# Optimization experiments

Hardware: AMD Instinct MI355X
Metric: run time of the kernel (lower is better)

## Reference

```python
import jax, jax.numpy as jnp
import numpy as np

RHO = 0.5
SIGMA = 0.3
BATCH = 32768
L = 1024

# Concrete drifts (abstract in the original base class): classic linear filtering pair
# b(x, y) = -x  (mean-reverting state drift), B(x, y) = x (observation drift = state)
def _b(x, y):
    return -x

def _B(x, y):
    return x


def setup_inputs() -> dict:
    key = jax.random.key(0)
    k1, k2, k3 = jax.random.split(key, 3)
    x0 = jax.random.normal(k1, (BATCH,), dtype=jnp.float32)
    y0 = jax.random.normal(k2, (BATCH,), dtype=jnp.float32)
    ts = (jnp.arange(L, dtype=jnp.float32) / (L - 1))  # uniform grid on [0, 1]
    z = jax.random.normal(k3, (L - 1, BATCH, 2), dtype=jnp.float32)
    return {"x0": x0, "y0": y0, "ts": ts, "z": z}


def reference(x0, y0, ts, z):
    hs = ts[1:] - ts[:-1]  # (L-1,)

    def step(carry, inp):
        x, y = carry
        h, zi = inp  # h scalar, zi (batch, 2)
        sqrt_h = jnp.sqrt(h)
        dW1 = sqrt_h * zi[:, 1]
        # faithful to source: dW[:,0] = rho^2*dW[:,0] + (1-rho^2)*dW[:,1]
        dW0 = RHO ** 2 * (sqrt_h * zi[:, 0]) + (1.0 - RHO ** 2) * dW1
        x_new = x + _b(x, y) * h + SIGMA * dW0
        # note: source updates x first, then uses the NEW x inside B
        y_new = y + _B(x_new, y) * h + dW1
        return (x_new, y_new), jnp.stack((x_new, y_new), axis=1)  # (batch, 2)

    (_, _), traj = jax.lax.scan(step, (x0, y0), (hs, z))  # traj: (L-1, batch, 2)
    xy0 = jnp.stack((x0, y0), axis=1)[None]  # (1, batch, 2)
    xy = jnp.concatenate([xy0, traj], axis=0)  # (L, batch, 2)
    return jnp.transpose(xy, (1, 0, 2))  # (batch, L, 2)
```

## Files before the change

kernel.cpp:

```cpp
#include <hip/hip_runtime.h>

#define BATCH 32768
#define LEN   1024
#define TT    16
#define NTK   64
#define WV    8
#define PB    128

typedef float f32x4 __attribute__((ext_vector_type(4)));


__global__ __launch_bounds__(512, 2)
void sde_kernel(const float* __restrict__ x0,
                const float* __restrict__ y0,
                const float* __restrict__ ts,
                const float* __restrict__ z,
                float* __restrict__ out)
{
    const int tid  = threadIdx.x;
    const int lane = tid & 63;
    const int w    = tid >> 6;
    const int bb   = blockIdx.x * PB;

    __shared__ __align__(16) float2 ttile[WV][PB][18];
    __shared__ __align__(16) float2 arr[WV][PB];

    const float h  = (ts[LEN - 1] - ts[0]) * (1.0f / 1023.0f);
    const float q  = 1.0f - h;
    const float sh = sqrtf(h);
    const float Ax = 0.075f * sh;
    const float Bx = 0.225f * sh;
    const float q2 = q * q, q4 = q2 * q2, q8 = q4 * q4;
    const float ALPHA = q8 * q8;
    const float GAL   = q * (1.0f - ALPHA);
    const float l2q   = log2f(q);

    const int off = blockIdx.x & 7;
    const int NR  = off ? 9 : 8;

    const float2 xi = *(const float2*)&x0[bb + 2 * lane];
    const float2 yi = *(const float2*)&y0[bb + 2 * lane];

    const int   jloc = (2 * lane) & 15;
    const float a0 = exp2f((float)(jloc + 1) * l2q);
    const float a1 = a0 * q;
    const float g0 = q * (1.0f - a0);
    const float g1 = q * (1.0f - a1);
    const int   wt = lane >> 3;

    const float4* zb4 = (const float4*)z + (bb >> 1) + lane;

    float U0 = 0.f, V0 = 0.f, U1 = 0.f, V1 = 0.f;

    for (int r = 0; r < NR; ++r) {
        const int  k  = 8 * r + w - off;
        const bool kv = (unsigned)k < (unsigned)NTK;

        if (kv) {
            float4 zv[TT];
            const int rowb = 16 * k - 1;
#pragma unroll
            for (int j = 0; j < TT; ++j) {
                int row = rowb + j;
                row = row < 0 ? 0 : row;
                zv[j] = zb4[(size_t)row << 14];
            }
            float xa, ya, xb, yb;
            if (k == 0) { xa = xi.x; ya = yi.x; xb = xi.y; yb = yi.y; }
            else        { xa = 0.f;  ya = 0.f;  xb = 0.f;  yb = 0.f;  }
#pragma unroll
            for (int j = 0; j < TT; j += 2) {
                float2 pa0, pb0;
                if (j == 0 && k == 0) {
                    pa0 = make_float2(xa, ya); pb0 = make_float2(xb, yb);
                } else {
                    const float4 zi = zv[j];
                    xa = fmaf(xa, q, fmaf(Ax, zi.x, Bx * zi.y));
                    ya = ya + fmaf(xa, h, sh * zi.y);
                    xb = fmaf(xb, q, fmaf(Ax, zi.z, Bx * zi.w));
                    yb = yb + fmaf(xb, h, sh * zi.w);
                    pa0 = make_float2(xa, ya); pb0 = make_float2(xb, yb);
                }
                const float4 zi1 = zv[j + 1];
                xa = fmaf(xa, q, fmaf(Ax, zi1.x, Bx * zi1.y));
                ya = ya + fmaf(xa, h, sh * zi1.y);
                xb = fmaf(xb, q, fmaf(Ax, zi1.z, Bx * zi1.w));
                yb = yb + fmaf(xb, h, sh * zi1.w);
                *(float4*)&ttile[w][2 * lane    ][j] = make_float4(pa0.x, pa0.y, xa, ya);
                *(float4*)&ttile[w][2 * lane + 1][j] = make_float4(pb0.x, pb0.y, xb, yb);
            }
            *(float4*)&arr[w][2 * lane] = make_float4(xa, ya, xb, yb);
        }

        __syncthreads();

        if (w == 0) {
#pragma unroll
            for (int wp = 0; wp < WV; ++wp) {
                const int kp = 8 * r + wp - off;
                if ((unsigned)kp < (unsigned)NTK) {
                    const float4 s = *(const float4*)&arr[wp][2 * lane];
                    *(float4*)&arr[wp][2 * lane] = make_float4(U0, V0, U1, V1);
                    const float nU0 = fmaf(ALPHA, U0, s.x);
                    V0 = s.y + V0 + GAL * U0;  U0 = nU0;
                    const float nU1 = fmaf(ALPHA, U1, s.z);
                    V1 = s.w + V1 + GAL * U1;  U1 = nU1;
                }
            }
        }

        __syncthreads();

        {
            const int  kw = 8 * r + wt - off;
            const bool lv = (unsigned)kw < (unsigned)NTK;
            if (lv) {
                const int colf = (8 * r - off) * 32 + 4 * lane;
#pragma unroll
                for (int i = 0; i < 16; ++i) {
                    const int p = w * 16 + i;
                    const float4 t  = *(const float4*)&ttile[wt][p][jloc];
                    const float2 uv = arr[wt][p];
                    f32x4 o;
                    o.x = fmaf(uv.x, a0, t.x);
                    o.y = t.y + uv.y + uv.x * g0;
                    o.z = fmaf(uv.x, a1, t.z);
                    o.w = t.w + uv.y + uv.x * g1;
                    __builtin_nontemporal_store(o,
                        (f32x4*)&out[(size_t)(bb + p) * 2048 + colf]);
                }
            }
        }

        __syncthreads();
    }
}

extern "C" void kernel_launch(void* const* d_in, const int* in_sizes, int n_in,
                              void* d_out, int out_size, void* d_ws, size_t ws_size,
                              hipStream_t stream) {
    const float* x0 = (const float*)d_in[0];
    const float* y0 = (const float*)d_in[1];
    const float* ts = (const float*)d_in[2];
    const float* z  = (const float*)d_in[3];
    float* out = (float*)d_out;
    (void)d_ws; (void)ws_size; (void)in_sizes; (void)n_in; (void)out_size;

    sde_kernel<<<BATCH / PB, 512, 0, stream>>>(x0, y0, ts, z, out);
}
```

Measured before the change: 98.80 us.

## Double-buffer z prefetch across rounds and swizzle the LDS trajectory tile

Unrolls the round loop into nine fixed macro invocations. Each round now issues the next round's z loads into a second register buffer before computing the current one. Barriers only wait on LDS counters, so those global loads stay in flight across synchronisation. The shared trajectory tile uses an XOR swizzle on the column index to reduce bank conflicts on the transposed reads. The cost is roughly double the register footprint for z, under a 512x2 launch bound, which risks spills or lower occupancy.

```diff
diff --git a/kernel.cpp b/kernel.cpp
--- a/kernel.cpp
+++ b/kernel.cpp
@@ -9,6 +9,87 @@
 
 typedef float f32x4 __attribute__((ext_vector_type(4)));
 
+
+#define BAR() do { asm volatile("s_waitcnt lgkmcnt(0)" ::: "memory"); \
+                   __builtin_amdgcn_s_barrier(); } while (0)
+
+#define STEP(ZI) do { \
+    xa = fmaf(xa, q, fmaf(Ax, ZI.x, Bx * ZI.y)); \
+    ya = ya + fmaf(xa, h, sh * ZI.y); \
+    xb = fmaf(xb, q, fmaf(Ax, ZI.z, Bx * ZI.w)); \
+    yb = yb + fmaf(xb, h, sh * ZI.w); \
+} while (0)
+
+#define ROUND(R, CUR, NXT, PRE_, FIRST_) do { \
+    const int k_ = 8 * (R) + w - off; \
+    if (PRE_) {   \
+        const int kn_ = 8 * ((R) + 1) + w - off;    \
+        if ((unsigned)kn_ < (unsigned)NTK) { \
+            const int rowb_ = 16 * kn_ - 1; \
+            _Pragma("unroll") \
+            for (int j = 0; j < TT; ++j) \
+                NXT[j] = zb4[(size_t)(rowb_ + j) << 14]; \
+        } \
+    } \
+    if ((unsigned)k_ < (unsigned)NTK) { \
+        float xa, ya, xb, yb; \
+        if (FIRST_ && k_ == 0) { xa = xi.x; ya = yi.x; xb = xi.y; yb = yi.y; } \
+        else                   { xa = 0.f;  ya = 0.f;  xb = 0.f;  yb = 0.f;  } \
+        float* tb0_ = ttile + ((size_t)w * PB + 2 * lane) * 36; \
+        _Pragma("unroll") \
+        for (int j = 0; j < TT; j += 2) { \
+            float2 pa0_, pb0_; \
+            if (FIRST_ && k_ == 0 && j == 0) { \
+                pa0_ = make_float2(xa, ya); pb0_ = make_float2(xb, yb); \
+            } else { \
+                const float4 zi_ = CUR[j]; STEP(zi_); \
+                pa0_ = make_float2(xa, ya); pb0_ = make_float2(xb, yb); \
+            } \
+            const float4 zi1_ = CUR[j + 1]; STEP(zi1_); \
+            const int o_ = 4 * ((j >> 1) ^ csw); \
+            *(float4*)&tb0_[o_]      = make_float4(pa0_.x, pa0_.y, xa, ya); \
+            *(float4*)&tb0_[36 + o_] = make_float4(pb0_.x, pb0_.y, xb, yb); \
+        } \
+        *(float4*)&arr[w][4 * lane] = make_float4(xa, ya, xb, yb); \
+    } \
+    BAR();   \
+    if (w == 0) { \
+        _Pragma("unroll") \
+        for (int wp = 0; wp < WV; ++wp) { \
+            const int kp_ = 8 * (R) + wp - off; \
+            if ((unsigned)kp_ < (unsigned)NTK) { \
+                const float4 s_ = *(const float4*)&arr[wp][4 * lane]; \
+                *(float4*)&arr[wp][4 * lane] = make_float4(U0, V0, U1, V1); \
+                const float nU0_ = fmaf(ALPHA, U0, s_.x); \
+                V0 = s_.y + V0 + GAL * U0;  U0 = nU0_; \
+                const float nU1_ = fmaf(ALPHA, U1, s_.z); \
+                V1 = s_.w + V1 + GAL * U1;  U1 = nU1_; \
+            } \
+        } \
+    } \
+    BAR();   \
+    { \
+        const int kw_ = 8 * (R) + wt - off; \
+        if ((unsigned)kw_ < (unsigned)NTK) { \
+            const int colf_ = (8 * (R) - off) * 32 + 4 * lane; \
+            _Pragma("unroll") \
+            for (int i = 0; i < 16; ++i) { \
+                const int p_ = w * 16 + i; \
+                const float4 t_ = *(const float4*)&ttile[ \
+                    ((size_t)wt * PB + p_) * 36 + 4 * (csw ^ ((p_ >> 1) & 7))]; \
+                const float2 uv_ = *(const float2*)&arr[wt][2 * p_]; \
+                f32x4 o_; \
+                o_.x = fmaf(uv_.x, a0, t_.x); \
+                o_.y = t_.y + uv_.y + uv_.x * g0; \
+                o_.z = fmaf(uv_.x, a1, t_.z); \
+                o_.w = t_.w + uv_.y + uv_.x * g1; \
+                __builtin_nontemporal_store(o_, \
+                    (f32x4*)&out[(size_t)(bb + p_) * 2048 + colf_]); \
+            } \
+        } \
+    } \
+    BAR();   \
+} while (0)
 
 __global__ __launch_bounds__(512, 2)
 void sde_kernel(const float* __restrict__ x0,
@@ -22,8 +103,8 @@
     const int w    = tid >> 6;
     const int bb   = blockIdx.x * PB;
 
-    __shared__ __align__(16) float2 ttile[WV][PB][18];
-    __shared__ __align__(16) float2 arr[WV][PB];
+    __shared__ __align__(16) float ttile[WV * PB * 36];
+    __shared__ __align__(16) float arr[WV][260];
 
     const float h  = (ts[LEN - 1] - ts[0]) * (1.0f / 1023.0f);
     const float q  = 1.0f - h;
@@ -33,16 +114,15 @@
     const float q2 = q * q, q4 = q2 * q2, q8 = q4 * q4;
     const float ALPHA = q8 * q8;
     const float GAL   = q * (1.0f - ALPHA);
-    const float l2q   = log2f(q);
 
     const int off = blockIdx.x & 7;
-    const int NR  = off ? 9 : 8;
 
     const float2 xi = *(const float2*)&x0[bb + 2 * lane];
     const float2 yi = *(const float2*)&y0[bb + 2 * lane];
 
+    const int   csw  = lane & 7;
     const int   jloc = (2 * lane) & 15;
-    const float a0 = exp2f((float)(jloc + 1) * l2q);
+    const float a0 = exp2f((float)(jloc + 1) * log2f(q));
     const float a1 = a0 * q;
     const float g0 = q * (1.0f - a0);
     const float g1 = q * (1.0f - a1);
@@ -52,88 +132,30 @@
 
     float U0 = 0.f, V0 = 0.f, U1 = 0.f, V1 = 0.f;
 
-    for (int r = 0; r < NR; ++r) {
-        const int  k  = 8 * r + w - off;
-        const bool kv = (unsigned)k < (unsigned)NTK;
+    float4 zvA[TT], zvB[TT];
 
-        if (kv) {
-            float4 zv[TT];
-            const int rowb = 16 * k - 1;
+    {
+        const int k0 = w - off;
+        if ((unsigned)k0 < (unsigned)NTK) {
+            const int rowb = 16 * k0 - 1;
 #pragma unroll
             for (int j = 0; j < TT; ++j) {
                 int row = rowb + j;
                 row = row < 0 ? 0 : row;
-                zv[j] = zb4[(size_t)row << 14];
-            }
-            float xa, ya, xb, yb;
-            if (k == 0) { xa = xi.x; ya = yi.x; xb = xi.y; yb = yi.y; }
-            else        { xa = 0.f;  ya = 0.f;  xb = 0.f;  yb = 0.f;  }
-#pragma unroll
-            for (int j = 0; j < TT; j += 2) {
-                float2 pa0, pb0;
-                if (j == 0 && k == 0) {
-                    pa0 = make_float2(xa, ya); pb0 = make_float2(xb, yb);
-                } else {
-                    const float4 zi = zv[j];
-                    xa = fmaf(xa, q, fmaf(Ax, zi.x, Bx * zi.y));
-                    ya = ya + fmaf(xa, h, sh * zi.y);
-                    xb = fmaf(xb, q, fmaf(Ax, zi.z, Bx * zi.w));
-                    yb = yb + fmaf(xb, h, sh * zi.w);
-                    pa0 = make_float2(xa, ya); pb0 = make_float2(xb, yb);
-                }
-                const float4 zi1 = zv[j + 1];
-                xa = fmaf(xa, q, fmaf(Ax, zi1.x, Bx * zi1.y));
-                ya = ya + fmaf(xa, h, sh * zi1.y);
-                xb = fmaf(xb, q, fmaf(Ax, zi1.z, Bx * zi1.w));
-                yb = yb + fmaf(xb, h, sh * zi1.w);
-                *(float4*)&ttile[w][2 * lane    ][j] = make_float4(pa0.x, pa0.y, xa, ya);
-                *(float4*)&ttile[w][2 * lane + 1][j] = make_float4(pb0.x, pb0.y, xb, yb);
-            }
-            *(float4*)&arr[w][2 * lane] = make_float4(xa, ya, xb, yb);
-        }
-
-        __syncthreads();
-
-        if (w == 0) {
-#pragma unroll
-            for (int wp = 0; wp < WV; ++wp) {
-                const int kp = 8 * r + wp - off;
-                if ((unsigned)kp < (unsigned)NTK) {
-                    const float4 s = *(const float4*)&arr[wp][2 * lane];
-                    *(float4*)&arr[wp][2 * lane] = make_float4(U0, V0, U1, V1);
-                    const float nU0 = fmaf(ALPHA, U0, s.x);
-                    V0 = s.y + V0 + GAL * U0;  U0 = nU0;
-                    const float nU1 = fmaf(ALPHA, U1, s.z);
-                    V1 = s.w + V1 + GAL * U1;  U1 = nU1;
-                }
+                zvA[j] = zb4[(size_t)row << 14];
             }
         }
+    }
 
-        __syncthreads();
-
-        {
-            const int  kw = 8 * r + wt - off;
-            const bool lv = (unsigned)kw < (unsigned)NTK;
-            if (lv) {
-                const int colf = (8 * r - off) * 32 + 4 * lane;
-#pragma unroll
-                for (int i = 0; i < 16; ++i) {
-                    const int p = w * 16 + i;
-                    const float4 t  = *(const float4*)&ttile[wt][p][jloc];
-                    const float2 uv = arr[wt][p];
-                    f32x4 o;
-                    o.x = fmaf(uv.x, a0, t.x);
-                    o.y = t.y + uv.y + uv.x * g0;
-                    o.z = fmaf(uv.x, a1, t.z);
-                    o.w = t.w + uv.y + uv.x * g1;
-                    __builtin_nontemporal_store(o,
-                        (f32x4*)&out[(size_t)(bb + p) * 2048 + colf]);
-                }
-            }
-        }
-
-        __syncthreads();
-    }
+    ROUND(0, zvA, zvB, 1, 1);
+    ROUND(1, zvB, zvA, 1, 0);
+    ROUND(2, zvA, zvB, 1, 0);
+    ROUND(3, zvB, zvA, 1, 0);
+    ROUND(4, zvA, zvB, 1, 0);
+    ROUND(5, zvB, zvA, 1, 0);
+    ROUND(6, zvA, zvB, 1, 0);
+    ROUND(7, zvB, zvA, 1, 0);
+    ROUND(8, zvA, zvB, 0, 0);
 }
 
 extern "C" void kernel_launch(void* const* d_in, const int* in_sizes, int n_in,
```

Result: faster. 92.22 us (median of 2 runs) (-6.7%).
